# Optimization experiments

Hardware: AMD Instinct MI355X
Metric: run time of the kernel (lower is better)

## Reference

```python
import jax, jax.numpy as jnp
import numpy as np
import math

D_MODEL = 1024
NUM_HEADS = 16
D_K = D_MODEL // NUM_HEADS
SEQ = 4096
THETA = 10000.0


def _rope_tables(d_k, max_seq_len, theta):
    freqs = 1.0 / theta ** (jnp.arange(0, d_k, 2, dtype=jnp.float32) / d_k)  # (d_k/2,)
    pos = jnp.arange(max_seq_len, dtype=jnp.float32)
    ang = pos[:, None] * freqs[None, :]  # (S, d_k/2)
    return jnp.cos(ang), jnp.sin(ang)


def setup_inputs() -> dict:
    key = jax.random.key(0)
    ks = jax.random.split(key, 5)
    std = math.sqrt(2.0 / (D_MODEL + D_MODEL))
    def trunc_w(k):
        return jax.random.truncated_normal(k, -3.0, 3.0, (D_MODEL, D_MODEL), jnp.float32) * std
    x = jax.random.normal(ks[0], (1, SEQ, D_MODEL), jnp.float32)
    Wq, Wk, Wv, Wo = trunc_w(ks[1]), trunc_w(ks[2]), trunc_w(ks[3]), trunc_w(ks[4])
    cos, sin = _rope_tables(D_K, SEQ, THETA)
    positions = jnp.arange(SEQ, dtype=jnp.int32)
    return {"x": x, "Wq": Wq, "Wk": Wk, "Wv": Wv, "Wo": Wo,
            "cos": cos, "sin": sin, "positions": positions}


def _apply_rope(t, cos, sin, positions):
    # t: (b, h, s, d_k); cos/sin: (max_s, d_k/2)
    c = cos[positions][None, None]  # (1,1,s,d_k/2)
    s = sin[positions][None, None]
    x1, x2 = t[..., ::2], t[..., 1::2]
    rotated = jnp.stack([x1 * c - x2 * s, x1 * s + x2 * c], axis=-1)  # (b,h,s,d_k/2,2)
    return rotated.reshape(t.shape)


def reference(x, Wq, Wk, Wv, Wo, cos, sin, positions):
    b, s, d = x.shape
    h, dk = NUM_HEADS, D_K
    def proj(W):
        y = jnp.einsum('bsi,oi->bso', x, W)
        return y.reshape(b, s, h, dk).transpose(0, 2, 1, 3)  # (b,h,s,dk)
    Q, K, V = proj(Wq), proj(Wk), proj(Wv)
    Q = _apply_rope(Q, cos, sin, positions)
    K = _apply_rope(K, cos, sin, positions)
    scores = jnp.einsum('bhqd,bhkd->bhqk', Q, K) / math.sqrt(dk)
    causal = jnp.tril(jnp.ones((s, s), dtype=bool))
    scores = jnp.where(causal[None, None], scores, -jnp.inf)
    weights = jax.nn.softmax(scores, axis=-1)
    y = jnp.einsum('bhqk,bhkd->bhqd', weights, V)
    y = y.transpose(0, 2, 1, 3).reshape(b, s, d)
    return jnp.einsum('bsi,oi->bso', y, Wo)
```

## Files before the change

kernel.cpp:

```cpp
#include <hip/hip_runtime.h>
#include <math.h>

#define SEQ 4096
#define DM  1024
#define NH  16
#define DK  64

typedef __attribute__((ext_vector_type(4))) float f32x4;
typedef __attribute__((ext_vector_type(8))) short bf16x8;
typedef __attribute__((ext_vector_type(8))) unsigned short u16x8;

union FragU { u16x8 u; bf16x8 b; ushort4 q[2]; unsigned w[4]; };

__device__ __forceinline__ unsigned cvtpk(float a, float b) {
    unsigned r; asm("v_cvt_pk_bf16_f32 %0, %1, %2" : "=v"(r) : "v"(a), "v"(b)); return r;
}
__device__ __forceinline__ float fexp2(float x) {
    float r; asm("v_exp_f32 %0, %1" : "=v"(r) : "v"(x)); return r;
}
__device__ __forceinline__ void split4(float4 v, ushort4& hv, ushort4& lv) {
    union { ushort4 q; unsigned w[2]; } H, L;
    H.w[0] = cvtpk(v.x, v.y); H.w[1] = cvtpk(v.z, v.w);
    const float rx = v.x - __uint_as_float(H.w[0] << 16);
    const float ry = v.y - __uint_as_float(H.w[0] & 0xffff0000u);
    const float rz = v.z - __uint_as_float(H.w[1] << 16);
    const float rw = v.w - __uint_as_float(H.w[1] & 0xffff0000u);
    L.w[0] = cvtpk(rx, ry); L.w[1] = cvtpk(rz, rw);
    hv = H.q; lv = L.q;
}
__device__ __forceinline__ void split1(float f, unsigned short& h, unsigned short& l) {
    const unsigned hw = cvtpk(f, f) & 0xffffu;
    h = (unsigned short)hw;
    const float r = f - __uint_as_float(hw << 16);
    l = (unsigned short)(__float_as_uint(r) >> 16);
}

template<int MODE>
__global__ __launch_bounds__(256, 2)
void gemm_mfma(const float* __restrict__ Af,
               const unsigned short* __restrict__ Ahi, const unsigned short* __restrict__ Alo,
               const float* __restrict__ W0, const float* __restrict__ W1,
               const float* __restrict__ W2,
               unsigned short* __restrict__ OQh, unsigned short* __restrict__ OQl,
               unsigned short* __restrict__ OKh, unsigned short* __restrict__ OKl,
               unsigned short* __restrict__ OVh, unsigned short* __restrict__ OVl,
               float* __restrict__ Ofp,
               const float* __restrict__ cosT, const float* __restrict__ sinT,
               const int* __restrict__ positions)
{
    constexpr int NT = (MODE == 4) ? 24 : 8;
    __shared__ unsigned short As[128][76];
    __shared__ unsigned short Bs[128][76];

    const int t   = threadIdx.x;
    const int bid = blockIdx.x;
    const int qpx = (32 * NT) >> 3;
    const int swz = (bid & 7) * qpx + (bid >> 3);
    const int by  = swz / NT;
    const int bxf = swz % NT;
    const int wt  = (MODE == 4) ? (bxf >> 3) : 0;
    const int bx  = (MODE == 4) ? (bxf & 7) : bxf;
    const int m0  = by * 128;
    const float* W = (MODE == 4) ? (wt == 0 ? W0 : (wt == 1 ? W1 : W2)) : W0;

    const int lane = t & 63, w = t >> 6;
    const int wr = w >> 1, wc = w & 1;
    const int l15 = lane & 15, lg = lane >> 4;

    const int ar = t >> 1, ah = t & 1;
    const float* Ap = (MODE == 4) ? &Af[(size_t)(m0 + ar) * DM + ah * 16] : nullptr;
    const unsigned short* Aph = (MODE == 0) ? &Ahi[(size_t)(m0 + ar) * DM + ah * 16] : nullptr;
    const unsigned short* Apl = (MODE == 0) ? &Alo[(size_t)(m0 + ar) * DM + ah * 16] : nullptr;
    const float* Wp = &W[(size_t)(bx * 128 + ar) * DM + ah * 16];

    f32x4 acc[4][4];
#pragma unroll
    for (int mi = 0; mi < 4; ++mi)
#pragma unroll
        for (int ni = 0; ni < 4; ++ni) acc[mi][ni] = (f32x4){0.f, 0.f, 0.f, 0.f};

    float4 pa[4], pb[4];
    u16x8 pah[2], pal[2];
    if constexpr (MODE == 4) {
#pragma unroll
        for (int g = 0; g < 4; ++g) pa[g] = *reinterpret_cast<const float4*>(Ap + g * 4);
    } else {
        pah[0] = *reinterpret_cast<const u16x8*>(Aph);
        pah[1] = *reinterpret_cast<const u16x8*>(Aph + 8);
        pal[0] = *reinterpret_cast<const u16x8*>(Apl);
        pal[1] = *reinterpret_cast<const u16x8*>(Apl + 8);
    }
#pragma unroll
    for (int g = 0; g < 4; ++g) pb[g] = *reinterpret_cast<const float4*>(Wp + g * 4);

    for (int kt = 0; kt < 32; ++kt) {
        if constexpr (MODE == 4) {
#pragma unroll
            for (int g = 0; g < 4; ++g) {
                ushort4 hv, lv;
                split4(pa[g], hv, lv);
                *reinterpret_cast<ushort4*>(&As[ar][8 * g + 4 * ah])      = hv;
                *reinterpret_cast<ushort4*>(&As[ar][32 + 8 * g + 4 * ah]) = lv;
            }
        } else {
            FragU h0, h1, l0, l1;
            h0.u = pah[0]; h1.u = pah[1]; l0.u = pal[0]; l1.u = pal[1];
            *reinterpret_cast<ushort4*>(&As[ar][0  + 4 * ah]) = h0.q[0];
            *reinterpret_cast<ushort4*>(&As[ar][8  + 4 * ah]) = h0.q[1];
            *reinterpret_cast<ushort4*>(&As[ar][16 + 4 * ah]) = h1.q[0];
            *reinterpret_cast<ushort4*>(&As[ar][24 + 4 * ah]) = h1.q[1];
            *reinterpret_cast<ushort4*>(&As[ar][32 + 4 * ah]) = l0.q[0];
            *reinterpret_cast<ushort4*>(&As[ar][40 + 4 * ah]) = l0.q[1];
            *reinterpret_cast<ushort4*>(&As[ar][48 + 4 * ah]) = l1.q[0];
            *reinterpret_cast<ushort4*>(&As[ar][56 + 4 * ah]) = l1.q[1];
        }
#pragma unroll
        for (int g = 0; g < 4; ++g) {
            ushort4 hv, lv;
            split4(pb[g], hv, lv);
            *reinterpret_cast<ushort4*>(&Bs[ar][8 * g + 4 * ah])      = hv;
            *reinterpret_cast<ushort4*>(&Bs[ar][32 + 8 * g + 4 * ah]) = lv;
        }
        __syncthreads();

        if (kt < 31) {
            const int ko = (kt + 1) * 32;
            if constexpr (MODE == 4) {
#pragma unroll
                for (int g = 0; g < 4; ++g)
                    pa[g] = *reinterpret_cast<const float4*>(Ap + ko + g * 4);
            } else {
                pah[0] = *reinterpret_cast<const u16x8*>(Aph + ko);
                pah[1] = *reinterpret_cast<const u16x8*>(Aph + ko + 8);
                pal[0] = *reinterpret_cast<const u16x8*>(Apl + ko);
                pal[1] = *reinterpret_cast<const u16x8*>(Apl + ko + 8);
            }
#pragma unroll
            for (int g = 0; g < 4; ++g)
                pb[g] = *reinterpret_cast<const float4*>(Wp + ko + g * 4);
        }

        FragU b_h[4], b_l[4];
#pragma unroll
        for (int ni = 0; ni < 4; ++ni) {
            const int row = wc * 64 + ni * 16 + l15;
            b_h[ni].u = *reinterpret_cast<const u16x8*>(&Bs[row][8 * lg]);
            b_l[ni].u = *reinterpret_cast<const u16x8*>(&Bs[row][32 + 8 * lg]);
        }
#pragma unroll
        for (int mi = 0; mi < 4; ++mi) {
            FragU a_h, a_l;
            const int row = wr * 64 + mi * 16 + l15;
            a_h.u = *reinterpret_cast<const u16x8*>(&As[row][8 * lg]);
            a_l.u = *reinterpret_cast<const u16x8*>(&As[row][32 + 8 * lg]);
#pragma unroll
            for (int ni = 0; ni < 4; ++ni) {
                f32x4 c = acc[mi][ni];
                c = __builtin_amdgcn_mfma_f32_16x16x32_bf16(a_h.b, b_h[ni].b, c, 0, 0, 0);
                c = __builtin_amdgcn_mfma_f32_16x16x32_bf16(a_h.b, b_l[ni].b, c, 0, 0, 0);
                c = __builtin_amdgcn_mfma_f32_16x16x32_bf16(a_l.b, b_h[ni].b, c, 0, 0, 0);
                acc[mi][ni] = c;
            }
        }
        __syncthreads();
    }

    if constexpr (MODE == 0) {
#pragma unroll
        for (int mi = 0; mi < 4; ++mi)
#pragma unroll
            for (int ni = 0; ni < 4; ++ni)
#pragma unroll
                for (int r = 0; r < 4; ++r) {
                    const int m = m0 + wr * 64 + mi * 16 + lg * 4 + r;
                    const int n = bx * 128 + wc * 64 + ni * 16 + l15;
                    Ofp[(size_t)m * DM + n] = acc[mi][ni][r];
                }
    } else if (wt == 2) {
#pragma unroll
        for (int mi = 0; mi < 4; ++mi)
#pragma unroll
            for (int ni = 0; ni < 4; ++ni) {
                ushort4 hv, lv;
                unsigned short* hp = (unsigned short*)&hv;
                unsigned short* lp = (unsigned short*)&lv;
#pragma unroll
                for (int r = 0; r < 4; ++r) split1(acc[mi][ni][r], hp[r], lp[r]);
                const int vrow = bx * 128 + wc * 64 + ni * 16 + l15;
                const size_t off = (size_t)vrow * SEQ + m0 + wr * 64 + mi * 16 + lg * 4;
                *reinterpret_cast<ushort4*>(&OVh[off]) = hv;
                *reinterpret_cast<ushort4*>(&OVl[off]) = lv;
            }
    } else {
        unsigned short* Oh = (wt == 0) ? OQh : OKh;
        unsigned short* Ol = (wt == 0) ? OQl : OKl;
        const int head = bx * 2 + wc;
        const float qsc = 0.1803368801f;
#pragma unroll
        for (int mi = 0; mi < 4; ++mi)
#pragma unroll
            for (int r = 0; r < 4; ++r) {
                const int m   = m0 + wr * 64 + mi * 16 + lg * 4 + r;
                const int pos = positions[m];
#pragma unroll
                for (int ni = 0; ni < 4; ++ni) {
                    float val = acc[mi][ni][r];
                    const int d = ni * 16 + l15;
                    const float other = __shfl_xor(val, 1);
                    const float cc = cosT[pos * 32 + ni * 8 + (l15 >> 1)];
                    const float ss = sinT[pos * 32 + ni * 8 + (l15 >> 1)];
                    val = (d & 1) ? fmaf(other, ss, val * cc)
                                  : fmaf(other, -ss, val * cc);
                    if (wt == 0) val *= qsc;
                    unsigned short hh, ll;
                    split1(val, hh, ll);
                    const size_t off = ((size_t)head * SEQ + m) * DK + d;
                    Oh[off] = hh; Ol[off] = ll;
                }
            }
    }
}

__global__ __launch_bounds__(256, 1)
void attn_mfma(const unsigned short* __restrict__ Qhi, const unsigned short* __restrict__ Qlo,
               const unsigned short* __restrict__ Khi, const unsigned short* __restrict__ Klo,
               const unsigned short* __restrict__ Vhi,
               unsigned short* __restrict__ Yh, unsigned short* __restrict__ Yl)
{
    __shared__ unsigned short KsH[64][64], KsL[64][64], Vs[64][64];

    const int t = threadIdx.x, lane = t & 63, w = t >> 6;
    const int bid = blockIdx.x;
    const int xcd = bid & 7, j = bid >> 3;
    const int h  = 2 * xcd + (j & 1);
    const int qt = 15 - (j >> 1);
    const int l15 = lane & 15, lg = lane >> 4, dg = lg * 4;
    const int srow = t >> 2, q16 = t & 3;

    int wcol[4];
#pragma unroll
    for (int m = 0; m < 4; ++m) {
        const int g = (q16 >> 1) * 4 + m;
        wcol[m] = (((g ^ (srow & 7)) << 3) + ((q16 & 1) << 2));
    }

    const int NKT    = 4 * qt + 4;
    const int diagkt = 4 * qt + w;

    bf16x8 qh[4][2], ql[4][2];
#pragma unroll
    for (int u = 0; u < 4; ++u) {
        const size_t qrow = ((size_t)h * SEQ + (size_t)qt * 256 + w * 64 + u * 16 + l15) * DK;
#pragma unroll
        for (int c = 0; c < 2; ++c) {
            FragU uh, ul;
            uh.q[0] = *reinterpret_cast<const ushort4*>(&Qhi[qrow + c * 32 + dg]);
            uh.q[1] = *reinterpret_cast<const ushort4*>(&Qhi[qrow + c * 32 + 16 + dg]);
            ul.q[0] = *reinterpret_cast<const ushort4*>(&Qlo[qrow + c * 32 + dg]);
            ul.q[1] = *reinterpret_cast<const ushort4*>(&Qlo[qrow + c * 32 + 16 + dg]);
            qh[u][c] = uh.b; ql[u][c] = ul.b;
        }
    }

    f32x4 yacc[4][4];
#pragma unroll
    for (int u = 0; u < 4; ++u)
#pragma unroll
        for (int dt = 0; dt < 4; ++dt) yacc[u][dt] = (f32x4){0.f, 0.f, 0.f, 0.f};
    float m_run[4] = {-1e30f, -1e30f, -1e30f, -1e30f};
    float l_run[4] = {0.f, 0.f, 0.f, 0.f};

    u16x8 pf[6];
    {
        const size_t gK = ((size_t)h * SEQ + srow) * DK + q16 * 16;
        const size_t gV = ((size_t)h * DK + srow) * SEQ + q16 * 16;
        pf[0] = *reinterpret_cast<const u16x8*>(&Khi[gK]);
        pf[1] = *reinterpret_cast<const u16x8*>(&Khi[gK + 8]);
        pf[2] = *reinterpret_cast<const u16x8*>(&Klo[gK]);
        pf[3] = *reinterpret_cast<const u16x8*>(&Klo[gK + 8]);
        pf[4] = *reinterpret_cast<const u16x8*>(&Vhi[gV]);
        pf[5] = *reinterpret_cast<const u16x8*>(&Vhi[gV + 8]);
    }

    for (int kt = 0; kt < NKT; ++kt) {
        __syncthreads();
        {
            FragU f;
            f.u = pf[0];
            *reinterpret_cast<ushort4*>(&KsH[srow][wcol[0]]) = f.q[0];
            *reinterpret_cast<ushort4*>(&KsH[srow][wcol[1]]) = f.q[1];
            f.u = pf[1];
            *reinterpret_cast<ushort4*>(&KsH[srow][wcol[2]]) = f.q[0];
            *reinterpret_cast<ushort4*>(&KsH[srow][wcol[3]]) = f.q[1];
            f.u = pf[2];
            *reinterpret_cast<ushort4*>(&KsL[srow][wcol[0]]) = f.q[0];
            *reinterpret_cast<ushort4*>(&KsL[srow][wcol[1]]) = f.q[1];
            f.u = pf[3];
            *reinterpret_cast<ushort4*>(&KsL[srow][wcol[2]]) = f.q[0];
            *reinterpret_cast<ushort4*>(&KsL[srow][wcol[3]]) = f.q[1];
            f.u = pf[4];
            *reinterpret_cast<ushort4*>(&Vs[srow][wcol[0]]) = f.q[0];
            *reinterpret_cast<ushort4*>(&Vs[srow][wcol[1]]) = f.q[1];
            f.u = pf[5];
            *reinterpret_cast<ushort4*>(&Vs[srow][wcol[2]]) = f.q[0];
            *reinterpret_cast<ushort4*>(&Vs[srow][wcol[3]]) = f.q[1];
        }
        __syncthreads();

        if (kt + 1 < NKT) {
            const size_t gK = ((size_t)h * SEQ + (size_t)(kt + 1) * 64 + srow) * DK + q16 * 16;
            const size_t gV = ((size_t)h * DK + srow) * SEQ + (size_t)(kt + 1) * 64 + q16 * 16;
            pf[0] = *reinterpret_cast<const u16x8*>(&Khi[gK]);
            pf[1] = *reinterpret_cast<const u16x8*>(&Khi[gK + 8]);
            pf[2] = *reinterpret_cast<const u16x8*>(&Klo[gK]);
            pf[3] = *reinterpret_cast<const u16x8*>(&Klo[gK + 8]);
            pf[4] = *reinterpret_cast<const u16x8*>(&Vhi[gV]);
            pf[5] = *reinterpret_cast<const u16x8*>(&Vhi[gV + 8]);
        }

        if (kt > diagkt) continue;
        const bool diag = (kt == diagkt);

        f32x4 st[4][4];
        __builtin_amdgcn_s_setprio(1);
#pragma unroll
        for (int ktile = 0; ktile < 4; ++ktile) {
            const int rowK = ktile * 16 + l15;
            const int swk  = rowK & 7;
            FragU kh0, kl0, kh1, kl1;
            {
                const int p0 = ((0 + lg) ^ swk) << 3;
                const int p1 = ((4 + lg) ^ swk) << 3;
                kh0.u = *reinterpret_cast<const u16x8*>(&KsH[rowK][p0]);
                kl0.u = *reinterpret_cast<const u16x8*>(&KsL[rowK][p0]);
                kh1.u = *reinterpret_cast<const u16x8*>(&KsH[rowK][p1]);
                kl1.u = *reinterpret_cast<const u16x8*>(&KsL[rowK][p1]);
            }
#pragma unroll
            for (int u = 0; u < 4; ++u) {
                if (diag && ktile > u) {
                    st[u][ktile] = (f32x4){-1e30f, -1e30f, -1e30f, -1e30f};
                    continue;
                }
                f32x4 s = (f32x4){0.f, 0.f, 0.f, 0.f};
                s = __builtin_amdgcn_mfma_f32_16x16x32_bf16(kh0.b, qh[u][0], s, 0, 0, 0);
                s = __builtin_amdgcn_mfma_f32_16x16x32_bf16(kh0.b, ql[u][0], s, 0, 0, 0);
                s = __builtin_amdgcn_mfma_f32_16x16x32_bf16(kl0.b, qh[u][0], s, 0, 0, 0);
                s = __builtin_amdgcn_mfma_f32_16x16x32_bf16(kh1.b, qh[u][1], s, 0, 0, 0);
                s = __builtin_amdgcn_mfma_f32_16x16x32_bf16(kh1.b, ql[u][1], s, 0, 0, 0);
                s = __builtin_amdgcn_mfma_f32_16x16x32_bf16(kl1.b, qh[u][1], s, 0, 0, 0);
                st[u][ktile] = s;
            }
        }
        __builtin_amdgcn_s_setprio(0);

        if (diag) {
#pragma unroll
            for (int u = 0; u < 4; ++u)
#pragma unroll
                for (int r = 0; r < 4; ++r)
                    if (dg + r > l15) st[u][u][r] = -1e30f;
        }

        bf16x8 pa[4][2];
#pragma unroll
        for (int u = 0; u < 4; ++u) {
            float rowmax = st[u][0][0];
#pragma unroll
            for (int ktile = 0; ktile < 4; ++ktile)
#pragma unroll
                for (int r = 0; r < 4; ++r) rowmax = fmaxf(rowmax, st[u][ktile][r]);
            rowmax = fmaxf(rowmax, __shfl_xor(rowmax, 16));
            rowmax = fmaxf(rowmax, __shfl_xor(rowmax, 32));
            if (!__all(rowmax <= m_run[u] + 11.5f)) {
                const float mnew = fmaxf(m_run[u], rowmax);
                const float factor = fexp2(m_run[u] - mnew);
                l_run[u] *= factor;
#pragma unroll
                for (int r = 0; r < 4; ++r) {
                    const float fr = __shfl(factor, (lg << 2) | r);
#pragma unroll
                    for (int dt = 0; dt < 4; ++dt) yacc[u][dt][r] *= fr;
                }
                m_run[u] = mnew;
            }
            float p[4][4]; float psum = 0.f;
#pragma unroll
            for (int ktile = 0; ktile < 4; ++ktile)
#pragma unroll
                for (int r = 0; r < 4; ++r) {
                    p[ktile][r] = fexp2(st[u][ktile][r] - m_run[u]);
                    psum += p[ktile][r];
                }
            psum += __shfl_xor(psum, 16);
            psum += __shfl_xor(psum, 32);
            l_run[u] += psum;
#pragma unroll
            for (int c = 0; c < 2; ++c) {
                FragU P;
                P.w[0] = cvtpk(p[2 * c][0],     p[2 * c][1]);
                P.w[1] = cvtpk(p[2 * c][2],     p[2 * c][3]);
                P.w[2] = cvtpk(p[2 * c + 1][0], p[2 * c + 1][1]);
                P.w[3] = cvtpk(p[2 * c + 1][2], p[2 * c + 1][3]);
                pa[u][c] = P.b;
            }
        }

        __builtin_amdgcn_s_setprio(1);
#pragma unroll
        for (int dt = 0; dt < 4; ++dt) {
            const int rowV = dt * 16 + l15;
            const int swv  = rowV & 7;
#pragma unroll
            for (int c = 0; c < 2; ++c) {
                FragU vh;
                vh.u = *reinterpret_cast<const u16x8*>(&Vs[rowV][((c * 4 + lg) ^ swv) << 3]);
#pragma unroll
                for (int u = 0; u < 4; ++u) {
                    if (diag && c > (u >> 1)) continue;
                    yacc[u][dt] = __builtin_amdgcn_mfma_f32_16x16x32_bf16(pa[u][c], vh.b, yacc[u][dt], 0, 0, 0);
                }
            }
        }
        __builtin_amdgcn_s_setprio(0);
    }

#pragma unroll
    for (int u = 0; u < 4; ++u) {
        const float inv = 1.0f / l_run[u];
#pragma unroll
        for (int r = 0; r < 4; ++r) {
            const float ir = __shfl(inv, (lg << 2) | r);
            const size_t row = (size_t)qt * 256 + w * 64 + u * 16 + lg * 4 + r;
#pragma unroll
            for (int dt = 0; dt < 4; ++dt) {
                unsigned short hh, ll;
                split1(yacc[u][dt][r] * ir, hh, ll);
                const size_t off = row * DM + h * DK + dt * 16 + l15;
                Yh[off] = hh; Yl[off] = ll;
            }
        }
    }
}

extern "C" void kernel_launch(void* const* d_in, const int* in_sizes, int n_in,
                              void* d_out, int out_size, void* d_ws, size_t ws_size,
                              hipStream_t stream)
{
    const float* x    = (const float*)d_in[0];
    const float* Wq   = (const float*)d_in[1];
    const float* Wk   = (const float*)d_in[2];
    const float* Wv   = (const float*)d_in[3];
    const float* Wo   = (const float*)d_in[4];
    const float* cosT = (const float*)d_in[5];
    const float* sinT = (const float*)d_in[6];
    const int*   pos  = (const int*)d_in[7];
    float* out = (float*)d_out;

    const size_t E = (size_t)SEQ * DM;
    unsigned short* qh = (unsigned short*)d_ws;
    unsigned short* ql = qh + E;
    unsigned short* kh = ql + E;
    unsigned short* kl = kh + E;
    unsigned short* vh = kl + E;
    unsigned short* vl = vh + E;
    unsigned short* yh = vl + E;
    unsigned short* yl = yh + E;

    gemm_mfma<4><<<dim3(768), dim3(256), 0, stream>>>(
        x, nullptr, nullptr, Wq, Wk, Wv,
        qh, ql, kh, kl, vh, vl, nullptr, cosT, sinT, pos);
    attn_mfma<<<dim3(256), dim3(256), 0, stream>>>(qh, ql, kh, kl, vh, yh, yl);
    gemm_mfma<0><<<dim3(256), dim3(256), 0, stream>>>(
        nullptr, yh, yl, Wo, nullptr, nullptr,
        nullptr, nullptr, nullptr, nullptr, nullptr, nullptr, out, cosT, sinT, pos);
}
```

Measured before the change: 320.1 us.

## Halve attention query tile to 128 rows, launch 512 blocks with causal pairing

The attention kernel now processes 128 query rows per block instead of 256, with each wave handling 32 rows. The grid doubles to 512 blocks and launch bounds allow two blocks per CU. The block-to-tile mapping pairs long and short causal query tiles per head to balance work across CUs. This adds parallelism and occupancy, but K/V tiles are reloaded by twice as many blocks and each K/V load is amortized over fewer query rows.

Result: faster. 291.6 us (-8.9%).

```diff
diff --git a/kernel.cpp b/kernel.cpp
--- a/kernel.cpp
+++ b/kernel.cpp
@@ -221,7 +221,7 @@
     }
 }
 
-__global__ __launch_bounds__(256, 1)
+__global__ __launch_bounds__(256, 2)
 void attn_mfma(const unsigned short* __restrict__ Qhi, const unsigned short* __restrict__ Qlo,
                const unsigned short* __restrict__ Khi, const unsigned short* __restrict__ Klo,
                const unsigned short* __restrict__ Vhi,
@@ -231,11 +231,16 @@
 
     const int t = threadIdx.x, lane = t & 63, w = t >> 6;
     const int bid = blockIdx.x;
-    const int xcd = bid & 7, j = bid >> 3;
-    const int h  = 2 * xcd + (j & 1);
-    const int qt = 15 - (j >> 1);
+    const int xcd = bid & 7;
+    const int s   = bid >> 3;
+    const int i_  = s >> 1, hl = s & 1;
+    const int A   = (i_ < 16) ? i_ : 47 - i_;
+    const int qt  = hl ? (31 - A) : A;
+    const int h   = 2 * xcd + hl;
+
     const int l15 = lane & 15, lg = lane >> 4, dg = lg * 4;
     const int srow = t >> 2, q16 = t & 3;
+    const int wh = w & 1;
 
     int wcol[4];
 #pragma unroll
@@ -244,13 +249,13 @@
         wcol[m] = (((g ^ (srow & 7)) << 3) + ((q16 & 1) << 2));
     }
 
-    const int NKT    = 4 * qt + 4;
-    const int diagkt = 4 * qt + w;
-
-    bf16x8 qh[4][2], ql[4][2];
-#pragma unroll
-    for (int u = 0; u < 4; ++u) {
-        const size_t qrow = ((size_t)h * SEQ + (size_t)qt * 256 + w * 64 + u * 16 + l15) * DK;
+    const int NKT    = 2 * qt + 2;
+    const int diagkt = 2 * qt + (w >> 1);
+
+    bf16x8 qh[2][2], ql[2][2];
+#pragma unroll
+    for (int u = 0; u < 2; ++u) {
+        const size_t qrow = ((size_t)h * SEQ + (size_t)qt * 128 + w * 32 + u * 16 + l15) * DK;
 #pragma unroll
         for (int c = 0; c < 2; ++c) {
             FragU uh, ul;
@@ -262,13 +267,12 @@
         }
     }
 
-    f32x4 yacc[4][4];
-#pragma unroll
-    for (int u = 0; u < 4; ++u)
+    f32x4 yacc[2][4];
+#pragma unroll
+    for (int u = 0; u < 2; ++u)
 #pragma unroll
         for (int dt = 0; dt < 4; ++dt) yacc[u][dt] = (f32x4){0.f, 0.f, 0.f, 0.f};
-    float m_run[4] = {-1e30f, -1e30f, -1e30f, -1e30f};
-    float l_run[4] = {0.f, 0.f, 0.f, 0.f};
+    float m_run[2] = {-1e30f, -1e30f}, l_run[2] = {0.f, 0.f};
 
     u16x8 pf[6];
     {
@@ -321,7 +325,7 @@
         if (kt > diagkt) continue;
         const bool diag = (kt == diagkt);
 
-        f32x4 st[4][4];
+        f32x4 st[2][4];
         __builtin_amdgcn_s_setprio(1);
 #pragma unroll
         for (int ktile = 0; ktile < 4; ++ktile) {
@@ -337,34 +341,36 @@
                 kl1.u = *reinterpret_cast<const u16x8*>(&KsL[rowK][p1]);
             }
 #pragma unroll
-            for (int u = 0; u < 4; ++u) {
-                if (diag && ktile > u) {
+            for (int u = 0; u < 2; ++u) {
+                if (diag && ktile > wh * 2 + u) {
                     st[u][ktile] = (f32x4){-1e30f, -1e30f, -1e30f, -1e30f};
                     continue;
                 }
-                f32x4 s = (f32x4){0.f, 0.f, 0.f, 0.f};
-                s = __builtin_amdgcn_mfma_f32_16x16x32_bf16(kh0.b, qh[u][0], s, 0, 0, 0);
-                s = __builtin_amdgcn_mfma_f32_16x16x32_bf16(kh0.b, ql[u][0], s, 0, 0, 0);
-                s = __builtin_amdgcn_mfma_f32_16x16x32_bf16(kl0.b, qh[u][0], s, 0, 0, 0);
-                s = __builtin_amdgcn_mfma_f32_16x16x32_bf16(kh1.b, qh[u][1], s, 0, 0, 0);
-                s = __builtin_amdgcn_mfma_f32_16x16x32_bf16(kh1.b, ql[u][1], s, 0, 0, 0);
-                s = __builtin_amdgcn_mfma_f32_16x16x32_bf16(kl1.b, qh[u][1], s, 0, 0, 0);
-                st[u][ktile] = s;
+                f32x4 s0 = (f32x4){0.f, 0.f, 0.f, 0.f};
+                s0 = __builtin_amdgcn_mfma_f32_16x16x32_bf16(kh0.b, qh[u][0], s0, 0, 0, 0);
+                s0 = __builtin_amdgcn_mfma_f32_16x16x32_bf16(kh0.b, ql[u][0], s0, 0, 0, 0);
+                s0 = __builtin_amdgcn_mfma_f32_16x16x32_bf16(kl0.b, qh[u][0], s0, 0, 0, 0);
+                s0 = __builtin_amdgcn_mfma_f32_16x16x32_bf16(kh1.b, qh[u][1], s0, 0, 0, 0);
+                s0 = __builtin_amdgcn_mfma_f32_16x16x32_bf16(kh1.b, ql[u][1], s0, 0, 0, 0);
+                s0 = __builtin_amdgcn_mfma_f32_16x16x32_bf16(kl1.b, qh[u][1], s0, 0, 0, 0);
+                st[u][ktile] = s0;
             }
         }
         __builtin_amdgcn_s_setprio(0);
 
         if (diag) {
 #pragma unroll
-            for (int u = 0; u < 4; ++u)
+            for (int u = 0; u < 2; ++u) {
+                const int ub = wh * 2 + u;
 #pragma unroll
                 for (int r = 0; r < 4; ++r)
-                    if (dg + r > l15) st[u][u][r] = -1e30f;
-        }
-
-        bf16x8 pa[4][2];
-#pragma unroll
-        for (int u = 0; u < 4; ++u) {
+                    if (dg + r > l15) st[u][ub][r] = -1e30f;
+            }
+        }
+
+        bf16x8 pa[2][2];
+#pragma unroll
+        for (int u = 0; u < 2; ++u) {
             float rowmax = st[u][0][0];
 #pragma unroll
             for (int ktile = 0; ktile < 4; ++ktile)
@@ -416,8 +422,8 @@
                 FragU vh;
                 vh.u = *reinterpret_cast<const u16x8*>(&Vs[rowV][((c * 4 + lg) ^ swv) << 3]);
 #pragma unroll
-                for (int u = 0; u < 4; ++u) {
-                    if (diag && c > (u >> 1)) continue;
+                for (int u = 0; u < 2; ++u) {
+                    if (diag && c == 1 && (wh * 2 + u) < 2) continue;
                     yacc[u][dt] = __builtin_amdgcn_mfma_f32_16x16x32_bf16(pa[u][c], vh.b, yacc[u][dt], 0, 0, 0);
                 }
             }
@@ -426,12 +432,12 @@
     }
 
 #pragma unroll
-    for (int u = 0; u < 4; ++u) {
+    for (int u = 0; u < 2; ++u) {
         const float inv = 1.0f / l_run[u];
 #pragma unroll
         for (int r = 0; r < 4; ++r) {
             const float ir = __shfl(inv, (lg << 2) | r);
-            const size_t row = (size_t)qt * 256 + w * 64 + u * 16 + lg * 4 + r;
+            const size_t row = (size_t)qt * 128 + w * 32 + u * 16 + lg * 4 + r;
 #pragma unroll
             for (int dt = 0; dt < 4; ++dt) {
                 unsigned short hh, ll;
@@ -470,7 +476,7 @@
     gemm_mfma<4><<<dim3(768), dim3(256), 0, stream>>>(
         x, nullptr, nullptr, Wq, Wk, Wv,
         qh, ql, kh, kl, vh, vl, nullptr, cosT, sinT, pos);
-    attn_mfma<<<dim3(256), dim3(256), 0, stream>>>(qh, ql, kh, kl, vh, yh, yl);
+    attn_mfma<<<dim3(512), dim3(256), 0, stream>>>(qh, ql, kh, kl, vh, yh, yl);
     gemm_mfma<0><<<dim3(256), dim3(256), 0, stream>>>(
         nullptr, yh, yl, Wo, nullptr, nullptr,
         nullptr, nullptr, nullptr, nullptr, nullptr, nullptr, out, cosT, sinT, pos);
```
